# Optimization experiments

Hardware: AMD Instinct MI355X
Metric: run time of the kernel (lower is better)

The kernel has to match this reference:

```python
import jax, jax.numpy as jnp
import numpy as np

EMBED_DIM = 1024
NUM_HEADS = 16
HEAD_DIM = EMBED_DIM // NUM_HEADS
SCALING = HEAD_DIM ** -0.5


def setup_inputs() -> dict:
    key = jax.random.key(0)
    ks = jax.random.split(key, 10)
    B, T, D = 4, 2048, EMBED_DIM
    s = 0.02
    return {
        "hidden_states": jax.random.normal(ks[0], (B, T, D), jnp.float32),
        "attention_mask": jnp.zeros((B, 1, T, T), jnp.float32),
        "Wq": jax.random.normal(ks[1], (D, D), jnp.float32) * s,
        "bq": jnp.zeros((D,), jnp.float32),
        "Wk": jax.random.normal(ks[2], (D, D), jnp.float32) * s,
        "bk": jnp.zeros((D,), jnp.float32),
        "Wv": jax.random.normal(ks[3], (D, D), jnp.float32) * s,
        "bv": jnp.zeros((D,), jnp.float32),
        "Wo": jax.random.normal(ks[4], (D, D), jnp.float32) * s,
        "bo": jnp.zeros((D,), jnp.float32),
    }


def reference(hidden_states, attention_mask, Wq, bq, Wk, bk, Wv, bv, Wo, bo):
    B, T, D = hidden_states.shape
    H, Hd = NUM_HEADS, HEAD_DIM
    # projections (torch Linear: x @ W.T + b; here W stored as (D_in, D_out))
    q = (hidden_states @ Wq + bq) * SCALING
    k = hidden_states @ Wk + bk
    v = hidden_states @ Wv + bv
    q = q.reshape(B, T, H, Hd).transpose(0, 2, 1, 3)  # [B,H,T,Hd]
    k = k.reshape(B, T, H, Hd).transpose(0, 2, 1, 3)
    v = v.reshape(B, T, H, Hd).transpose(0, 2, 1, 3)
    # eager attention: full [B,H,T,T] scores + additive mask + softmax
    scores = jnp.einsum("bhtd,bhsd->bhts", q, k)
    scores = scores + attention_mask[:, :, :, : k.shape[2]]
    attn_weights = jax.nn.softmax(scores, axis=-1)
    attn_output = jnp.einsum("bhts,bhsd->bhtd", attn_weights, v)
    attn_output = attn_output.transpose(0, 2, 1, 3).reshape(B, T, D)
    attn_output = attn_output @ Wo + bo
    return attn_output
```

## Files before the change

### kernel.cpp

```cpp
#include <hip/hip_runtime.h>
#include <hip/hip_bf16.h>
#include <cstdint>

#define TT 2048
#define DD 1024
#define NH 16
#define HD 64
#define NB 4
#define SCALING 0.125f
#define LOG2E 1.44269504088896340736f
#define QSCALE (0.125f * 1.44269504088896340736f)

typedef __bf16 bf16;
typedef __attribute__((ext_vector_type(8))) __bf16 bf16x8;
typedef __attribute__((ext_vector_type(4))) __bf16 bf16x4;
typedef __attribute__((ext_vector_type(4))) float f32x4;

__device__ __forceinline__ void gload_lds16(const bf16* g, bf16* l) {
    __builtin_amdgcn_global_load_lds(
        (__attribute__((address_space(1))) const void*)g,
        (__attribute__((address_space(3))) void*)l, 16, 0, 0);
}

__global__ __launch_bounds__(256) void k_prep(const float* __restrict__ x, bf16* __restrict__ xb,
                                              const float* __restrict__ Wq, const float* __restrict__ Wk,
                                              const float* __restrict__ Wv, const float* __restrict__ Wo,
                                              bf16* __restrict__ Wt) {
    __shared__ float tile_s[32][33];
    int bid = blockIdx.x, tid = threadIdx.x;
    if (bid < 8192) {
        size_t i = ((size_t)bid * 256 + tid) * 4;
        float4 v = *(const float4*)(x + i);
        bf16x4 o;
        o[0] = (bf16)v.x; o[1] = (bf16)v.y; o[2] = (bf16)v.z; o[3] = (bf16)v.w;
        *(bf16x4*)(xb + i) = o;
        return;
    }
    int b2 = bid - 8192;
    int mat = b2 >> 10, tl = b2 & 1023;
    int n0 = (tl & 31) * 32, k0 = (tl >> 5) * 32;
    const float* w = mat == 0 ? Wq : (mat == 1 ? Wk : (mat == 2 ? Wv : Wo));
    int tx = tid & 31, ty = tid >> 5;
#pragma unroll
    for (int i = 0; i < 4; i++)
        tile_s[ty + 8 * i][tx] = w[(size_t)(k0 + ty + 8 * i) * DD + n0 + tx];
    __syncthreads();
#pragma unroll
    for (int i = 0; i < 4; i++)
        Wt[(size_t)mat * DD * DD + (size_t)(n0 + ty + 8 * i) * DD + k0 + tx] = (bf16)tile_s[tx][ty + 8 * i];
}

__device__ __forceinline__ void gemm128_main(const bf16* __restrict__ A, const bf16* __restrict__ Bt,
                                             int m0, int n0, int K,
                                             bf16* smem, f32x4 acc[4][4]) {
    const int tid = threadIdx.x;
    const int w = tid >> 6, lane = tid & 63;
    const int wr = w >> 1, wc = w & 1, quad = lane >> 4, l16 = lane & 15;
    f32x4 zero = {0.f, 0.f, 0.f, 0.f};
#pragma unroll
    for (int mi = 0; mi < 4; mi++)
#pragma unroll
        for (int ni = 0; ni < 4; ni++) acc[mi][ni] = zero;

    int cidx[2], arow[2], kc[2];
#pragma unroll
    for (int j = 0; j < 2; j++) {
        int idx = w * 128 + j * 64 + lane;
        cidx[j] = idx * 8;
        arow[j] = idx >> 2;
        kc[j] = (idx & 3) * 8;
    }
    const bf16* Ab = A + (size_t)m0 * K;
    const bf16* Bb = Bt + (size_t)n0 * K;

#pragma unroll
    for (int j = 0; j < 2; j++) {
        gload_lds16(Ab + (size_t)arow[j] * K + kc[j], smem + cidx[j]);
        gload_lds16(Bb + (size_t)arow[j] * K + kc[j], smem + 4096 + cidx[j]);
    }
    __syncthreads();

    const int NT = K >> 5;
    for (int kt = 0; kt < NT; kt++) {
        bf16* cur = smem + (kt & 1) * 8192;
        if (kt + 1 < NT) {
            bf16* nxt = smem + ((kt + 1) & 1) * 8192;
            int k0 = (kt + 1) * 32;
#pragma unroll
            for (int j = 0; j < 2; j++) {
                gload_lds16(Ab + (size_t)arow[j] * K + k0 + kc[j], nxt + cidx[j]);
                gload_lds16(Bb + (size_t)arow[j] * K + k0 + kc[j], nxt + 4096 + cidx[j]);
            }
        }
        bf16x8 af[4], bfv[4];
#pragma unroll
        for (int i = 0; i < 4; i++)
            af[i] = *(const bf16x8*)(cur + (wr * 64 + i * 16 + l16) * 32 + quad * 8);
#pragma unroll
        for (int i = 0; i < 4; i++)
            bfv[i] = *(const bf16x8*)(cur + 4096 + (wc * 64 + i * 16 + l16) * 32 + quad * 8);
#pragma unroll
        for (int mi = 0; mi < 4; mi++)
#pragma unroll
            for (int ni = 0; ni < 4; ni++)
                acc[mi][ni] = __builtin_amdgcn_mfma_f32_16x16x32_bf16(af[mi], bfv[ni], acc[mi][ni], 0, 0, 0);
        __syncthreads();
    }
}

__global__ __launch_bounds__(256) void k_gemm_qkv(const bf16* __restrict__ Xb, const bf16* __restrict__ Wt,
                                                  const float* __restrict__ bq, const float* __restrict__ bk,
                                                  const float* __restrict__ bv,
                                                  bf16* __restrict__ qb, bf16* __restrict__ kb,
                                                  bf16* __restrict__ vt,
                                                  const float* __restrict__ mask, int* __restrict__ flags) {
    __shared__ bf16 smem[16384];
    __shared__ int s_any[4];
    const int bid = blockIdx.x, tid = threadIdx.x;
    const int grp = bid / 7, rem = bid % 7;

    if (rem >= 3) {
        int fid = grp * 4 + (rem - 3);
        int st = fid & 31, tt = (fid >> 5) & 15, bbm = fid >> 9;
        const float* mp = mask + ((size_t)bbm * TT + tt * 128) * TT + st * 64;
        int c = (tid & 15) * 4;
        int r0 = tid >> 4;
        int any = 0;
        for (int r = r0; r < 128; r += 16) {
            float4 v = *(const float4*)(mp + (size_t)r * TT + c);
            any |= (v.x != 0.f) | (v.y != 0.f) | (v.z != 0.f) | (v.w != 0.f);
        }
        any = __any(any) ? 1 : 0;
        if ((tid & 63) == 0) s_any[tid >> 6] = any;
        __syncthreads();
        if (tid == 0)
            flags[(bbm * 16 + tt) * 32 + st] = s_any[0] | s_any[1] | s_any[2] | s_any[3];
        return;
    }

    int g = grp * 3 + rem;
    int bx = g % 24, by = g / 24;
    int m0 = by * 128, n0 = bx * 128;
    f32x4 acc[4][4];
    gemm128_main(Xb, Wt, m0, n0, DD, smem, acc);

    const int w = tid >> 6, lane = tid & 63;
    const int wr = w >> 1, wc = w & 1, quad = lane >> 4, l16 = lane & 15;
    const int which = n0 >> 10;
    const int bbk = m0 >> 11, tbase = m0 & 2047;

    if (which < 2) {
        const float* bias = which == 0 ? bq : bk;
#pragma unroll
        for (int mi = 0; mi < 4; mi++)
#pragma unroll
            for (int ni = 0; ni < 4; ni++) {
                int nn = (n0 & 1023) + wc * 64 + ni * 16 + l16;
                int h = nn >> 6, d = nn & 63;
                float bb_ = bias[nn];
#pragma unroll
                for (int r = 0; r < 4; r++) {
                    int t = tbase + wr * 64 + mi * 16 + quad * 4 + r;
                    float v = acc[mi][ni][r] + bb_;
                    if (which == 0)
                        qb[(((size_t)bbk * NH + h) * TT + t) * HD + d] = (bf16)(v * QSCALE);
                    else
                        kb[(((size_t)bbk * NH + h) * TT + t) * HD + d] = (bf16)v;
                }
            }
    } else {
        const int nn0 = n0 & 1023;
#pragma unroll
        for (int phase = 0; phase < 2; phase++) {
            __syncthreads();
            if (wc == phase) {
#pragma unroll
                for (int mi = 0; mi < 4; mi++)
#pragma unroll
                    for (int ni = 0; ni < 4; ni++) {
                        int nn_l = ni * 16 + l16;
                        float bb_ = bv[nn0 + phase * 64 + nn_l];
#pragma unroll
                        for (int r = 0; r < 4; r++)
                            smem[nn_l * 132 + wr * 64 + quad * 16 + mi * 4 + r] = (bf16)(acc[mi][ni][r] + bb_);
                    }
            }
            __syncthreads();
            int hh = (nn0 + phase * 64) >> 6;
#pragma unroll
            for (int i = 0; i < 4; i++) {
                int idx = i * 256 + tid;
                int rr = idx >> 4, cc = (idx & 15) * 8;
                bf16x8 vv = *(const bf16x8*)(smem + rr * 132 + cc);
                *(bf16x8*)(vt + (((size_t)bbk * NH + hh) * HD + rr) * TT + tbase + cc) = vv;
            }
        }
    }
}

__global__ __launch_bounds__(256, 4) void k_attn(const bf16* __restrict__ qb, const bf16* __restrict__ kb,
                                                 const bf16* __restrict__ vt, const float* __restrict__ mask,
                                                 const int* __restrict__ flags, bf16* __restrict__ ob) {
    __shared__ bf16 SB[4][4096];
    __shared__ int s_anyflag;

    const int tq0 = blockIdx.x * 128;
    const int h = blockIdx.y, bb = blockIdx.z;
    const int tid = threadIdx.x, w = tid >> 6, lane = tid & 63;
    const int quad = lane >> 4, l16 = lane & 15;

    const bf16* Qg = qb + (((size_t)bb * NH + h) * TT + tq0) * HD;
    const bf16* Kg = kb + ((size_t)bb * NH + h) * TT * HD;
    const bf16* Vg = vt + ((size_t)bb * NH + h) * HD * TT;

    int cidx[2], koff[2], voff[2];
#pragma unroll
    for (int j = 0; j < 2; j++) {
        int idx = (w * 2 + j) * 64 + lane;
        int row = idx >> 3, m = idx & 7;
        cidx[j] = idx * 8;
        koff[j] = row * HD + ((m ^ (row & 7)) * 8);
        voff[j] = row * TT + ((m ^ (row & 7)) * 8);
    }

#pragma unroll
    for (int j = 0; j < 4; j++) {
        int idx = (w * 4 + j) * 64 + lane;
        int row = idx >> 3, m = idx & 7;
        gload_lds16(Qg + row * HD + (m ^ (row & 7)) * 8, &SB[2][0] + idx * 8);
    }
#pragma unroll
    for (int j = 0; j < 2; j++) {
        gload_lds16(Kg + koff[j], SB[0] + cidx[j]);
        gload_lds16(Vg + voff[j], SB[1] + cidx[j]);
    }

    const int fbase = (bb * 16 + blockIdx.x) * 32;
    {
        int f0 = (tid < 32) ? flags[fbase + tid] : 0;
        if (tid < 64) { int a = __any(f0 != 0) ? 1 : 0; if (tid == 0) s_anyflag = a; }
    }

    bf16x8 ones;
#pragma unroll
    for (int i = 0; i < 8; i++) ones[i] = (bf16)1.0f;

    f32x4 oa[2][4];
    f32x4 lacc[2];
    f32x4 zero = {0.f, 0.f, 0.f, 0.f};
#pragma unroll
    for (int qi = 0; qi < 2; qi++) {
        lacc[qi] = zero;
#pragma unroll
        for (int ni = 0; ni < 4; ni++) oa[qi][ni] = zero;
    }

    __syncthreads();
    const int anyflag = s_anyflag;

    bf16x8 aq[2][2];
#pragma unroll
    for (int kd = 0; kd < 2; kd++) {
        const int csw = ((kd * 4 + quad) ^ (l16 & 7)) * 8;
#pragma unroll
        for (int qi = 0; qi < 2; qi++)
            aq[kd][qi] = *(const bf16x8*)(&SB[2][0] + (w * 32 + qi * 16 + l16) * 64 + csw);
    }

#define ATTN_COMPUTE(Ks, Vs, S0)                                                              \
    {                                                                                         \
        f32x4 st[4][2];                                                                       \
        _Pragma("unroll") for (int si = 0; si < 4; si++)                                      \
            _Pragma("unroll") for (int qi = 0; qi < 2; qi++) st[si][qi] = zero;               \
        _Pragma("unroll") for (int kd = 0; kd < 2; kd++) {                                    \
            const int csw = ((kd * 4 + quad) ^ (l16 & 7)) * 8;                                \
            bf16x8 kf[4];                                                                     \
            _Pragma("unroll") for (int si = 0; si < 4; si++)                                  \
                kf[si] = *(const bf16x8*)((Ks) + (si * 16 + l16) * 64 + csw);                 \
            _Pragma("unroll") for (int si = 0; si < 4; si++)                                  \
                _Pragma("unroll") for (int qi = 0; qi < 2; qi++)                              \
                    st[si][qi] = __builtin_amdgcn_mfma_f32_16x16x32_bf16(kf[si], aq[kd][qi],  \
                                                                        st[si][qi], 0, 0, 0);\
        }                                                                                     \
        if (anyflag && flags[fbase + ((S0) >> 6)]) {                                          \
            const float* mp = mask + ((size_t)bb * TT + tq0) * TT + (S0);                     \
            _Pragma("unroll") for (int si = 0; si < 4; si++)                                  \
                _Pragma("unroll") for (int qi = 0; qi < 2; qi++)                              \
                    _Pragma("unroll") for (int r = 0; r < 4; r++)                             \
                        st[si][qi][r] += mp[(size_t)(w * 32 + qi * 16 + l16) * TT             \
                                            + si * 16 + quad * 4 + r] * LOG2E;                \
        }                                                                                     \
        bf16 ep[4][2][4];                                                                     \
        _Pragma("unroll") for (int si = 0; si < 4; si++)                                      \
            _Pragma("unroll") for (int qi = 0; qi < 2; qi++)                                  \
                _Pragma("unroll") for (int r = 0; r < 4; r++)                                 \
                    ep[si][qi][r] = (bf16)exp2f(st[si][qi][r]);                               \
        _Pragma("unroll") for (int kk = 0; kk < 2; kk++) {                                    \
            bf16x8 ap[2];                                                                     \
            _Pragma("unroll") for (int qi = 0; qi < 2; qi++)                                  \
                _Pragma("unroll") for (int j = 0; j < 8; j++)                                 \
                    ap[qi][j] = ep[2 * kk + (j >> 2)][qi][j & 3];                             \
            bf16x8 bv8[4];                                                                    \
            _Pragma("unroll") for (int ni = 0; ni < 4; ni++)                                  \
                bv8[ni] = *(const bf16x8*)((Vs) + (ni * 16 + l16) * 64                        \
                                           + ((quad * 2 + kk) ^ (l16 & 7)) * 8);              \
            _Pragma("unroll") for (int qi = 0; qi < 2; qi++)                                  \
                lacc[qi] = __builtin_amdgcn_mfma_f32_16x16x32_bf16(ap[qi], ones, lacc[qi],    \
                                                                   0, 0, 0);                  \
            _Pragma("unroll") for (int qi = 0; qi < 2; qi++)                                  \
                _Pragma("unroll") for (int ni = 0; ni < 4; ni++)                              \
                    oa[qi][ni] = __builtin_amdgcn_mfma_f32_16x16x32_bf16(ap[qi], bv8[ni],     \
                                                                         oa[qi][ni], 0, 0, 0);\
        }                                                                                     \
    }

    ATTN_COMPUTE(SB[0], SB[1], 0)
    __syncthreads();
#pragma unroll
    for (int j = 0; j < 2; j++) {
        gload_lds16(Kg + 64 * HD + koff[j], SB[2] + cidx[j]);
        gload_lds16(Vg + 64 + voff[j], SB[3] + cidx[j]);
    }
    __syncthreads();

    for (int i = 1; i < 32; i++) {
        const int cur = i & 1, nxt = cur ^ 1;
        if (i < 31) {
            const int sn = (i + 1) * 64;
#pragma unroll
            for (int j = 0; j < 2; j++) {
                gload_lds16(Kg + sn * HD + koff[j], SB[2 * nxt] + cidx[j]);
                gload_lds16(Vg + sn + voff[j], SB[2 * nxt + 1] + cidx[j]);
            }
        }
        ATTN_COMPUTE(SB[2 * cur], SB[2 * cur + 1], i * 64)
        __syncthreads();
    }
#undef ATTN_COMPUTE

#pragma unroll
    for (int qi = 0; qi < 2; qi++)
#pragma unroll
        for (int r = 0; r < 4; r++) {
            float inv = 1.f / lacc[qi][r];
            int trow = tq0 + w * 32 + qi * 16 + quad * 4 + r;
#pragma unroll
            for (int ni = 0; ni < 4; ni++) {
                float v = oa[qi][ni][r] * inv;
                ob[((size_t)bb * TT + trow) * DD + h * HD + ni * 16 + l16] = (bf16)v;
            }
        }
}

__global__ __launch_bounds__(256) void k_gemm_out(const bf16* __restrict__ Ob, const bf16* __restrict__ Wot,
                                                  const float* __restrict__ bo, float* __restrict__ out) {
    __shared__ bf16 smem[16384];
    int m0 = blockIdx.y * 128, n0 = blockIdx.x * 128;
    f32x4 acc[4][4];
    gemm128_main(Ob, Wot, m0, n0, DD, smem, acc);

    const int tid = threadIdx.x, w = tid >> 6, lane = tid & 63;
    const int wr = w >> 1, wc = w & 1, quad = lane >> 4, l16 = lane & 15;
#pragma unroll
    for (int mi = 0; mi < 4; mi++)
#pragma unroll
        for (int ni = 0; ni < 4; ni++) {
            int gn = n0 + wc * 64 + ni * 16 + l16;
            float bb_ = bo[gn];
#pragma unroll
            for (int r = 0; r < 4; r++) {
                int gm = m0 + wr * 64 + mi * 16 + quad * 4 + r;
                out[(size_t)gm * DD + gn] = acc[mi][ni][r] + bb_;
            }
        }
}

extern "C" void kernel_launch(void* const* d_in, const int* in_sizes, int n_in,
                              void* d_out, int out_size, void* d_ws, size_t ws_size,
                              hipStream_t stream) {
    const float* hidden = (const float*)d_in[0];
    const float* mask   = (const float*)d_in[1];
    const float* Wq     = (const float*)d_in[2];
    const float* bq     = (const float*)d_in[3];
    const float* Wk     = (const float*)d_in[4];
    const float* bk     = (const float*)d_in[5];
    const float* Wv     = (const float*)d_in[6];
    const float* bv     = (const float*)d_in[7];
    const float* Wo     = (const float*)d_in[8];
    const float* bo     = (const float*)d_in[9];
    float* out = (float*)d_out;
    char* ws = (char*)d_ws;

    const size_t MB = 1024 * 1024;
    bf16* Xb   = (bf16*)(ws);
    bf16* Wt   = (bf16*)(ws + 16 * MB);
    bf16* qb   = (bf16*)(ws + 24 * MB);
    bf16* kb   = (bf16*)(ws + 40 * MB);
    bf16* vt   = (bf16*)(ws + 56 * MB);
    bf16* ob   = (bf16*)(ws + 72 * MB);
    int* flags = (int*)(ws + 88 * MB);

    hipLaunchKernelGGL(k_prep, dim3(12288), dim3(256), 0, stream, hidden, Xb, Wq, Wk, Wv, Wo, Wt);
    hipLaunchKernelGGL(k_gemm_qkv, dim3(3584), dim3(256), 0, stream, Xb, Wt, bq, bk, bv, qb, kb, vt, mask, flags);
    hipLaunchKernelGGL(k_attn, dim3(16, 16, 4), dim3(256), 0, stream, qb, kb, vt, mask, flags, ob);
    hipLaunchKernelGGL(k_gemm_out, dim3(8, 64), dim3(256), 0, stream, ob, Wt + (size_t)3 * DD * DD, bo, out);
}
```

Measured before the change: 380.3 us.

## Use XOR-swizzled BK=64 GEMM tiles and stage Q/K epilogue through LDS

The shared GEMM main loop now loads 64-wide K tiles into a single LDS buffer with an XOR swizzle on the 16-byte chunks. Fragment reads use the matching swizzle to avoid bank conflicts, and there are half as many barriers per K step. In exchange, the previous double-buffered prefetch is gone, so global loads no longer overlap with MFMA work. The Q/K epilogue now writes to padded LDS and then issues coalesced 16-byte global stores instead of scattered 2-byte stores.

```diff
diff --git a/kernel.cpp b/kernel.cpp
--- a/kernel.cpp
+++ b/kernel.cpp
@@ -62,49 +62,41 @@
 #pragma unroll
         for (int ni = 0; ni < 4; ni++) acc[mi][ni] = zero;
 
-    int cidx[2], arow[2], kc[2];
-#pragma unroll
-    for (int j = 0; j < 2; j++) {
-        int idx = w * 128 + j * 64 + lane;
+    int cidx[4], goff[4];
+#pragma unroll
+    for (int j = 0; j < 4; j++) {
+        int idx = (w * 4 + j) * 64 + lane;
+        int row = idx >> 3, m = idx & 7;
         cidx[j] = idx * 8;
-        arow[j] = idx >> 2;
-        kc[j] = (idx & 3) * 8;
+        goff[j] = row * K + (m ^ (row & 7)) * 8;
     }
     const bf16* Ab = A + (size_t)m0 * K;
     const bf16* Bb = Bt + (size_t)n0 * K;
 
-#pragma unroll
-    for (int j = 0; j < 2; j++) {
-        gload_lds16(Ab + (size_t)arow[j] * K + kc[j], smem + cidx[j]);
-        gload_lds16(Bb + (size_t)arow[j] * K + kc[j], smem + 4096 + cidx[j]);
-    }
-    __syncthreads();
-
-    const int NT = K >> 5;
-    for (int kt = 0; kt < NT; kt++) {
-        bf16* cur = smem + (kt & 1) * 8192;
-        if (kt + 1 < NT) {
-            bf16* nxt = smem + ((kt + 1) & 1) * 8192;
-            int k0 = (kt + 1) * 32;
-#pragma unroll
-            for (int j = 0; j < 2; j++) {
-                gload_lds16(Ab + (size_t)arow[j] * K + k0 + kc[j], nxt + cidx[j]);
-                gload_lds16(Bb + (size_t)arow[j] * K + k0 + kc[j], nxt + 4096 + cidx[j]);
-            }
-        }
-        bf16x8 af[4], bfv[4];
-#pragma unroll
-        for (int i = 0; i < 4; i++)
-            af[i] = *(const bf16x8*)(cur + (wr * 64 + i * 16 + l16) * 32 + quad * 8);
-#pragma unroll
-        for (int i = 0; i < 4; i++)
-            bfv[i] = *(const bf16x8*)(cur + 4096 + (wc * 64 + i * 16 + l16) * 32 + quad * 8);
-#pragma unroll
-        for (int mi = 0; mi < 4; mi++)
-#pragma unroll
-            for (int ni = 0; ni < 4; ni++)
-                acc[mi][ni] = __builtin_amdgcn_mfma_f32_16x16x32_bf16(af[mi], bfv[ni], acc[mi][ni], 0, 0, 0);
+    for (int k0 = 0; k0 < K; k0 += 64) {
+        if (k0) __syncthreads();
+#pragma unroll
+        for (int j = 0; j < 4; j++) {
+            gload_lds16(Ab + k0 + goff[j], smem + cidx[j]);
+            gload_lds16(Bb + k0 + goff[j], smem + 8192 + cidx[j]);
+        }
         __syncthreads();
+#pragma unroll
+        for (int kd = 0; kd < 2; kd++) {
+            const int csw = ((kd * 4 + quad) ^ (l16 & 7)) * 8;
+            bf16x8 af[4], bfv[4];
+#pragma unroll
+            for (int i = 0; i < 4; i++)
+                af[i] = *(const bf16x8*)(smem + (wr * 64 + i * 16 + l16) * 64 + csw);
+#pragma unroll
+            for (int i = 0; i < 4; i++)
+                bfv[i] = *(const bf16x8*)(smem + 8192 + (wc * 64 + i * 16 + l16) * 64 + csw);
+#pragma unroll
+            for (int mi = 0; mi < 4; mi++)
+#pragma unroll
+                for (int ni = 0; ni < 4; ni++)
+                    acc[mi][ni] = __builtin_amdgcn_mfma_f32_16x16x32_bf16(af[mi], bfv[ni], acc[mi][ni], 0, 0, 0);
+        }
     }
 }
 
@@ -148,28 +140,40 @@
     const int wr = w >> 1, wc = w & 1, quad = lane >> 4, l16 = lane & 15;
     const int which = n0 >> 10;
     const int bbk = m0 >> 11, tbase = m0 & 2047;
+    const int nn0 = n0 & 1023;
 
     if (which < 2) {
         const float* bias = which == 0 ? bq : bk;
-#pragma unroll
-        for (int mi = 0; mi < 4; mi++)
-#pragma unroll
-            for (int ni = 0; ni < 4; ni++) {
-                int nn = (n0 & 1023) + wc * 64 + ni * 16 + l16;
-                int h = nn >> 6, d = nn & 63;
-                float bb_ = bias[nn];
-#pragma unroll
-                for (int r = 0; r < 4; r++) {
-                    int t = tbase + wr * 64 + mi * 16 + quad * 4 + r;
-                    float v = acc[mi][ni][r] + bb_;
-                    if (which == 0)
-                        qb[(((size_t)bbk * NH + h) * TT + t) * HD + d] = (bf16)(v * QSCALE);
-                    else
-                        kb[(((size_t)bbk * NH + h) * TT + t) * HD + d] = (bf16)v;
-                }
-            }
+        bf16* dst = which == 0 ? qb : kb;
+        const float scl = which == 0 ? QSCALE : 1.0f;
+#pragma unroll
+        for (int phase = 0; phase < 2; phase++) {
+            __syncthreads();
+            if (wc == phase) {
+#pragma unroll
+                for (int mi = 0; mi < 4; mi++)
+#pragma unroll
+                    for (int ni = 0; ni < 4; ni++) {
+                        int d = ni * 16 + l16;
+                        float bb_ = bias[nn0 + phase * 64 + d];
+#pragma unroll
+                        for (int r = 0; r < 4; r++) {
+                            int t_l = wr * 64 + mi * 16 + quad * 4 + r;
+                            smem[t_l * 72 + d] = (bf16)((acc[mi][ni][r] + bb_) * scl);
+                        }
+                    }
+            }
+            __syncthreads();
+            int hh = (nn0 + phase * 64) >> 6;
+            bf16* dp = dst + (((size_t)bbk * NH + hh) * TT + tbase) * HD;
+#pragma unroll
+            for (int i = 0; i < 4; i++) {
+                int idx = i * 256 + tid;
+                int rr = idx >> 3, cc = (idx & 7) * 8;
+                *(bf16x8*)(dp + (size_t)rr * HD + cc) = *(const bf16x8*)(smem + rr * 72 + cc);
+            }
+        }
     } else {
-        const int nn0 = n0 & 1023;
 #pragma unroll
         for (int phase = 0; phase < 2; phase++) {
             __syncthreads();
```

After: 360.7 us. 5.1% less time.
